# Optimization experiments

Measured on AMD Instinct MI355X. Metric: run time of the kernel, lower is better.

The kernel has to match this reference:

```python
import jax, jax.numpy as jnp
import numpy as np
import math

S = 72; IMG_W = 640; IMG_H = 360; STRIDE = 16
IN_CH = 256; AFC = 64
FMAP_H = IMG_H // STRIDE  # 22
FMAP_W = IMG_W // STRIDE  # 40
N_OFFSETS = S
LEFT_ANGLES = [72., 60., 49., 39., 30., 22.]
RIGHT_ANGLES = [108., 120., 131., 141., 150., 158.]
BOTTOM_ANGLES = [165., 150., 141., 131., 120., 108., 100., 90., 80., 72., 60., 49., 39., 30., 15.]
BATCH = 8


def _gen_anchor(start, angle, cut):
    n = FMAP_H if cut else N_OFFSETS
    ys = np.linspace(1., 0., n)
    a = np.zeros(5 + n)
    sx, sy = start
    a[2] = 1. - sy
    a[3] = sx
    a[5:] = (sx + (1. - ys - 1. + sy) / math.tan(angle * math.pi / 180.)) * IMG_W
    return a


def _gen_side(angles, nb, x=None, y=None):
    if x is None:
        starts = [(xx, y) for xx in np.linspace(1., 0., nb)]
    else:
        starts = [(x, yy) for yy in np.linspace(1., 0., nb)]
    anc = np.stack([_gen_anchor(s, a, False) for s in starts for a in angles])
    cut = np.stack([_gen_anchor(s, a, True) for s in starts for a in angles])
    return anc, cut


def build_anchor_tables():
    la, lc = _gen_side(LEFT_ANGLES, 72, x=0.)
    ra, rc = _gen_side(RIGHT_ANGLES, 72, x=1.)
    ba, bc = _gen_side(BOTTOM_ANGLES, 128, y=1.)
    anchors = np.concatenate([la, ba, ra]).astype(np.float32)  # [P, 5+S]
    cuts = np.concatenate([lc, bc, rc])                        # [P, 5+fmap_h]
    xs = np.flip(np.round(cuts[:, 5:] / STRIDE), axis=1).astype(np.int64)
    cut_xs = np.clip(xs, 0, FMAP_W - 1).astype(np.int32)       # [P, fmap_h]
    invalid = (xs < 0) | (xs > FMAP_W)                         # faithful to original (> not >=)
    return anchors, cut_xs, invalid


def setup_inputs():
    key = jax.random.key(0)
    ks = jax.random.split(key, 6)
    anchors, cut_xs, invalid = build_anchor_tables()
    P = anchors.shape[0]  # 2784
    D = AFC * FMAP_H      # 1408
    s = 0.02
    return {
        "x": jax.random.normal(ks[0], (BATCH, IN_CH, FMAP_H, FMAP_W), jnp.float32),
        "conv_w": jax.random.normal(ks[1], (AFC, IN_CH), jnp.float32) * s,
        "conv_b": jnp.zeros((AFC,), jnp.float32),
        "att_w": jax.random.normal(ks[2], (P - 1, D), jnp.float32) * s,
        "att_b": jnp.zeros((P - 1,), jnp.float32),
        "cls_w": jax.random.normal(ks[3], (2, 2 * D), jnp.float32) * s,
        "cls_b": jnp.zeros((2,), jnp.float32),
        "so_w": jax.random.normal(ks[4], (1, 2 * D), jnp.float32) * s,
        "so_b": jnp.zeros((1,), jnp.float32),
        "reg_w": jax.random.normal(ks[5], (N_OFFSETS + 1, 2 * D), jnp.float32) * s,
        "reg_b": jnp.zeros((N_OFFSETS + 1,), jnp.float32),
        "anchors": jnp.asarray(anchors),
        "cut_xs": jnp.asarray(cut_xs),
        "invalid_mask": jnp.asarray(invalid),
    }


def reference(x, conv_w, conv_b, att_w, att_b, cls_w, cls_b, so_w, so_b, reg_w, reg_b, anchors, cut_xs, invalid_mask):
    B = x.shape[0]
    P, H = cut_xs.shape
    # 1x1 conv
    feat = jnp.einsum('bchw,oc->bohw', x, conv_w) + conv_b[None, :, None, None]
    # fused anchor feature gather: rois[b,p,c,h] = feat[b,c,h,cut_xs[p,h]]
    rois = feat[:, :, jnp.arange(H)[None, :], cut_xs]           # [B,C,P,H]
    rois = jnp.transpose(rois, (0, 2, 1, 3))                    # [B,P,C,H]
    rois = jnp.where(invalid_mask[None, :, None, :], 0., rois)
    D = rois.shape[2] * H
    baf = rois.reshape(B, P, D)
    scores = baf.reshape(B * P, D) @ att_w.T + att_b
    attention = jax.nn.softmax(scores, axis=1).reshape(B, P, P - 1)
    # off-diagonal scatter (replaces torch eye/nonzero trick): M[b,i,j]=attention[b,i,j'] for j!=i, diag 0
    i_idx = jnp.arange(P)[:, None]
    j_off = jnp.arange(P - 1)[None, :]
    tgt_j = jnp.where(j_off < i_idx, j_off, j_off + 1)          # [P,P-1]
    M = jnp.zeros((B, P, P), x.dtype).at[:, jnp.broadcast_to(i_idx, (P, P - 1)), tgt_j].set(attention)
    # (baf^T @ M^T)^T == M @ baf
    att_feats = jnp.einsum('bpq,bqd->bpd', M, baf)
    feats = jnp.concatenate([att_feats, baf], axis=2).reshape(B * P, 2 * D)
    cls = (feats @ cls_w.T + cls_b).reshape(B, P, 2)
    so = jax.nn.sigmoid(feats @ so_w.T + so_b).reshape(B, P, 1)
    reg = (feats @ reg_w.T + reg_b).reshape(B, P, N_OFFSETS + 1)
    anc = jnp.broadcast_to(anchors[None], (B, P, anchors.shape[1]))
    reg_proposals = jnp.concatenate([cls, (anc[:, :, 2:3] + so) * 0.5, anc[:, :, 3:4], anc[:, :, 4:] + reg], axis=2)
    return reg_proposals, M, feat
```

## Files before the change

### kernel.cpp

```cpp
#include <hip/hip_runtime.h>
#include <stdint.h>

#define PTOT 2784
#define PM1  2783
#define DDIM 1408
#define NB   8
#define ROWS 22272
#define KHEAD 2816
#define MROW 2816
#define BTROWS 1536

typedef __attribute__((ext_vector_type(8))) short bf16x8;
typedef __attribute__((ext_vector_type(4))) float f32x4;
typedef long i64f8;
typedef __attribute__((ext_vector_type(2))) long i64x2;

__device__ __forceinline__ short f2bf_rne(float x) {
    uint32_t u = __float_as_uint(x);
    u += 0x7fffu + ((u >> 16) & 1u);
    return (short)(u >> 16);
}
__device__ __forceinline__ float bf2f(short s) {
    return __uint_as_float((uint32_t)(unsigned short)s << 16);
}

__device__ __forceinline__ unsigned char f2e4m3(float x) {
    uint32_t u = __float_as_uint(x);
    uint32_t sgn = (u >> 24) & 0x80u;
    uint32_t ax = u & 0x7fffffffu;
    ax += 0x7ffffu + ((ax >> 20) & 1u);
    if (ax >= 0x43E80000u) return (unsigned char)(sgn | 0x7Eu);
    if (ax < 0x3C800000u) return (unsigned char)sgn;
    uint32_t e = (ax >> 23) - 120u;
    uint32_t m = (ax >> 20) & 7u;
    return (unsigned char)(sgn | (e << 3) | m);
}

__device__ __forceinline__ uint32_t kperm(uint32_t c) {
    return (c & ~63u) + (((c >> 3) & 3) << 4) + (((c >> 5) & 1) << 3) + (c & 7);
}

__device__ __forceinline__ void gld16(const void* g, void* l) {
    __builtin_amdgcn_global_load_lds(
        (const __attribute__((address_space(1))) void*)(uintptr_t)g,
        (__attribute__((address_space(3))) void*)(uint32_t)(uintptr_t)l,
        16, 0, 0);
}

#define VMW(N) asm volatile("s_waitcnt vmcnt(" #N ")" ::: "memory")

__global__ __launch_bounds__(256) void k_conv(
    const float* __restrict__ x, const float* __restrict__ w,
    const float* __restrict__ cb, float* __restrict__ feat) {
  __shared__ float xs[256 * 32];
  int b = blockIdx.x / 28;
  int t0 = (blockIdx.x % 28) * 32;
  int t = threadIdx.x;
  for (int i = t; i < 256 * 32; i += 256) {
    int c = i >> 5, pos = i & 31;
    int hw = t0 + pos;
    xs[i] = (hw < 880) ? x[((size_t)b * 256 + c) * 880 + hw] : 0.f;
  }
  __syncthreads();
  int o = t & 63, g = t >> 6;
  float acc[8];
#pragma unroll
  for (int pp = 0; pp < 8; ++pp) acc[pp] = cb[o];
  const float* wr = w + o * 256;
  for (int c = 0; c < 256; ++c) {
    float wv = wr[c];
#pragma unroll
    for (int pp = 0; pp < 8; ++pp) acc[pp] += wv * xs[c * 32 + g + pp * 4];
  }
#pragma unroll
  for (int pp = 0; pp < 8; ++pp) {
    int hw = t0 + g + pp * 4;
    if (hw < 880) feat[((size_t)b * 64 + o) * 880 + hw] = acc[pp];
  }
}

__global__ __launch_bounds__(256) void k_prep(
    const float* __restrict__ att_w, const float* __restrict__ cls_w,
    const float* __restrict__ so_w, const float* __restrict__ reg_w,
    const float* __restrict__ cls_b, const float* __restrict__ so_b,
    const float* __restrict__ reg_b,
    short* __restrict__ attw, short* __restrict__ wbf,
    float* __restrict__ bias80, float* __restrict__ M,
    unsigned char* __restrict__ Mbf8, unsigned char* __restrict__ bafT8,
    short* __restrict__ Msc) {
  const uint32_t n_attw = 2816u * DDIM;
  const uint32_t n_w = 80u * KHEAD;
  const uint32_t n_pa = (uint32_t)NB * MROW * 32;
  const uint32_t n_pb = (uint32_t)NB * BTROWS * 32;
  const uint32_t total = n_attw + n_w + 80 + ROWS + n_pa + n_pb;
  for (uint32_t i = blockIdx.x * 256 + threadIdx.x; i < total;
       i += gridDim.x * 256) {
    if (i < n_attw) {
      uint32_t j = i / DDIM, k = i - j * DDIM;
      float v = (j < PM1) ? att_w[(size_t)j * DDIM + k] : 0.f;
      attw[i] = f2bf_rne(v);
    } else if (i < n_attw + n_w) {
      uint32_t ii = i - n_attw;
      uint32_t n = ii / KHEAD, k = ii - n * KHEAD;
      float v = 0.f;
      if (n < 2) v = cls_w[n * KHEAD + k];
      else if (n == 2) v = so_w[k];
      else if (n < 76) v = reg_w[(size_t)(n - 3) * KHEAD + k];
      wbf[ii] = f2bf_rne(v);
    } else if (i < n_attw + n_w + 80) {
      uint32_t n = i - n_attw - n_w;
      float v = 0.f;
      if (n < 2) v = cls_b[n];
      else if (n == 2) v = so_b[0];
      else if (n < 76) v = reg_b[n - 3];
      bias80[n] = v;
    } else if (i < n_attw + n_w + 80 + ROWS) {
      uint32_t r = i - n_attw - n_w - 80;
      uint32_t p = r % PTOT;
      M[(size_t)r * PTOT + p] = -1e30f;
      if (Msc) Msc[(size_t)r * PTOT + p] = f2bf_rne(-1e30f);
    } else if (i < n_attw + n_w + 80 + ROWS + n_pa) {
      uint32_t ii = i - n_attw - n_w - 80 - ROWS;
      uint32_t row = ii >> 5; uint32_t c = ii & 31;
      Mbf8[(size_t)row * 2816 + kperm(2784 + c)] = 0;
    } else {
      uint32_t ii = i - n_attw - n_w - 80 - ROWS - n_pa;
      uint32_t row = ii >> 5; uint32_t c = ii & 31;
      bafT8[(size_t)row * 2816 + kperm(2784 + c)] = 0;
    }
  }
}

__global__ __launch_bounds__(256) void k_gather(
    const float* __restrict__ feat, const int* __restrict__ cutx,
    const unsigned char* __restrict__ inval,
    short* __restrict__ baf, unsigned char* __restrict__ bafT8) {
  int p0 = blockIdx.x * 64, d0 = blockIdx.y * 64, b = blockIdx.z;
  __shared__ short tile[64][72];
  int t = threadIdx.x;
  for (int i = t; i < 64 * 64; i += 256) {
    int pl = i >> 6, dl = i & 63;
    int p = p0 + pl, d = d0 + dl;
    float v = 0.f;
    if (p < PTOT && d < DDIM) {
      int c = d / 22, h = d - c * 22;
      if (!inval[p * 22 + h]) {
        int xc = cutx[p * 22 + h];
        v = feat[(((size_t)b * 64 + c) * 22 + h) * 40 + xc];
      }
    }
    tile[pl][dl] = f2bf_rne(v);
  }
  __syncthreads();
  if (d0 < DDIM) {
    for (int u = t; u < 512; u += 256) {
      int pl = u >> 3, dg = u & 7;
      int p = p0 + pl;
      if (p < PTOT) {
        bf16x8 v;
#pragma unroll
        for (int e = 0; e < 8; ++e) v[e] = tile[pl][dg * 8 + e];
        *(bf16x8*)&baf[((size_t)b * PTOT + p) * DDIM + d0 + dg * 8] = v;
      }
    }
  }
  for (int u = t; u < 512; u += 256) {
    int dl = u >> 3, pg = u & 7;
    int pbase = p0 + pg * 8;
    if (pbase + 7 < PTOT) {
      unsigned long long pk = 0;
#pragma unroll
      for (int e = 0; e < 8; ++e) {
        float fv = bf2f(tile[pg * 8 + e][dl]);
        pk |= (unsigned long long)f2e4m3(fv) << (8 * e);
      }
      *(unsigned long long*)&bafT8[((size_t)b * BTROWS + d0 + dl) * 2816 +
                                   kperm(pbase)] = pk;
    }
  }
}

#define SC_TILE(OFF_, S_, SN_, STAGE_, VM_)                                    \
  {                                                                            \
    const char* cb_ = sm + (S_) * 24576;                                       \
    if (STAGE_) {                                                              \
      char* nb_ = sm + (SN_) * 24576;                                          \
      gld16(gA0 + (OFF_), nb_ + ddA);                                          \
      gld16(gB0 + (OFF_), nb_ + 8192 + ddA);                                   \
      gld16(gB1 + (OFF_), nb_ + 16384 + ddA);                                  \
    }                                                                          \
    if ((VM_) == 6) VMW(6); else if ((VM_) == 3) VMW(3); else VMW(0);          \
    __builtin_amdgcn_s_barrier();                                              \
    bf16x8 av[4], bv[4];                                                       \
    _Pragma("unroll") for (int i = 0; i < 4; ++i)                              \
      av[i] = *(const bf16x8*)(cb_ + offA[i]);                                 \
    _Pragma("unroll") for (int i = 0; i < 4; ++i)                              \
      bv[i] = *(const bf16x8*)(cb_ + 8192 + offB[i]);                          \
    __builtin_amdgcn_s_setprio(1);                                             \
    _Pragma("unroll") for (int mi = 0; mi < 4; ++mi)                           \
      _Pragma("unroll") for (int ni = 0; ni < 4; ++ni)                         \
        acc[mi][ni] = __builtin_amdgcn_mfma_f32_16x16x32_bf16(                 \
            av[mi], bv[ni], acc[mi][ni], 0, 0, 0);                             \
    __builtin_amdgcn_s_setprio(0);                                             \
    __builtin_amdgcn_s_barrier();                                              \
  }

template<int OUTMODE>
__global__ __launch_bounds__(512, 4) void k_scores(
    const short* __restrict__ baf, const short* __restrict__ attw,
    const float* __restrict__ att_b, float* __restrict__ Mout,
    short* __restrict__ Msc) {
  __shared__ char sm[73728];
  int wg = blockIdx.x;
  int xcd = wg & 7, lin = wg >> 3;
  int wgid = (xcd < 2) ? xcd * 240 + lin : 480 + (xcd - 2) * 239 + lin;
  int it = wgid / 11, nt = wgid - it * 11;
  int m0 = it * 128, n0 = nt * 256;

  int t = threadIdx.x, w = t >> 6, l = t & 63;
  int lr = l & 15, lg = l >> 4;
  int wr = w >> 2, wc = w & 3;

  const char* gA0; const char* gB0; const char* gB1;
  int ddA = t * 16;
  {
    int oA = t * 16;
    int rA = oA >> 6, cA = (oA & 63) ^ (((oA >> 7) & 3) << 4);
    gA0 = (const char*)(baf + (size_t)(m0 + rA) * DDIM) + cA;
    int oB0 = t * 16;
    int rB0 = oB0 >> 6, cB0 = (oB0 & 63) ^ (((oB0 >> 7) & 3) << 4);
    gB0 = (const char*)(attw + (size_t)(n0 + rB0) * DDIM) + cB0;
    int oB1 = 8192 + t * 16;
    int rB1 = oB1 >> 6, cB1 = (oB1 & 63) ^ (((oB1 >> 7) & 3) << 4);
    gB1 = (const char*)(attw + (size_t)(n0 + rB1) * DDIM) + cB1;
  }
  int offA[4], offB[4];
#pragma unroll
  for (int i = 0; i < 4; ++i) {
    int xa = (wr * 64 + i * 16 + lr) * 64 + lg * 16;
    offA[i] = xa ^ (((xa >> 7) & 3) << 4);
    int xb = (wc * 64 + i * 16 + lr) * 64 + lg * 16;
    offB[i] = xb ^ (((xb >> 7) & 3) << 4);
  }

  f32x4 acc[4][4];
  const f32x4 fz = {0.f, 0.f, 0.f, 0.f};
#pragma unroll
  for (int mi = 0; mi < 4; ++mi)
#pragma unroll
    for (int ni = 0; ni < 4; ++ni) acc[mi][ni] = fz;

  gld16(gA0, sm + ddA);
  gld16(gB0, sm + 8192 + ddA);
  gld16(gB1, sm + 16384 + ddA);
  gld16(gA0 + 64, sm + 24576 + ddA);
  gld16(gB0 + 64, sm + 24576 + 8192 + ddA);
  gld16(gB1 + 64, sm + 24576 + 16384 + ddA);

  for (int q = 0; q < 14; ++q) {
    SC_TILE(128, 0, 2, 1, 6);
    SC_TILE(192, 1, 0, 1, 6);
    SC_TILE(256, 2, 1, 1, 6);
    gA0 += 192; gB0 += 192; gB1 += 192;
  }
  SC_TILE(0, 0, 0, 0, 3);
  SC_TILE(0, 1, 0, 0, 0);

#pragma unroll
  for (int mi = 0; mi < 4; ++mi) {
#pragma unroll
    for (int rg = 0; rg < 4; ++rg) {
      int gmi = m0 + wr * 64 + mi * 16 + lg * 4 + rg;
      int i = gmi % PTOT;
#pragma unroll
      for (int ni = 0; ni < 4; ++ni) {
        int j = n0 + wc * 64 + ni * 16 + lr;
        if (j < PM1) {
          int q2 = j + (j >= i);
          float v = acc[mi][ni][rg] + att_b[j];
          if (OUTMODE == 0) Mout[(size_t)gmi * PTOT + q2] = v;
          else              Msc[(size_t)gmi * PTOT + q2] = f2bf_rne(v);
        }
      }
    }
  }
}

#define AF_TILE(OFF_, S_, SN_, STAGE_, VM_)                                    \
  {                                                                            \
    const char* cb_ = sm + (S_) * 24576;                                       \
    if (STAGE_) {                                                              \
      char* nb_ = sm + (SN_) * 24576;                                          \
      gld16(gA0 + (OFF_), nb_ + ddA);                                          \
      gld16(gB0 + (OFF_), nb_ + 8192 + ddA);                                   \
      gld16(gB1 + (OFF_), nb_ + 16384 + ddA);                                  \
    }                                                                          \
    if ((VM_) == 6) VMW(6); else if ((VM_) == 3) VMW(3); else VMW(0);          \
    __builtin_amdgcn_s_barrier();                                              \
    i64x2 aw[4], bw[4];                                                        \
    _Pragma("unroll") for (int i = 0; i < 4; ++i)                              \
      aw[i] = *(const i64x2*)(cb_ + offA[i]);                                  \
    _Pragma("unroll") for (int i = 0; i < 4; ++i)                              \
      bw[i] = *(const i64x2*)(cb_ + 8192 + offB[i]);                           \
    __builtin_amdgcn_s_setprio(1);                                             \
    _Pragma("unroll") for (int ks = 0; ks < 2; ++ks)                           \
      _Pragma("unroll") for (int mi = 0; mi < 4; ++mi)                         \
        _Pragma("unroll") for (int ni = 0; ni < 4; ++ni)                       \
          acc[mi][ni] = __builtin_amdgcn_mfma_f32_16x16x32_fp8_fp8(            \
              aw[mi][ks], bw[ni][ks], acc[mi][ni], 0, 0, 0);                   \
    __builtin_amdgcn_s_setprio(0);                                             \
    __builtin_amdgcn_s_barrier();                                              \
  }

__global__ __launch_bounds__(512, 4) void k_attfeat8(
    const unsigned char* __restrict__ Mbf8,
    const unsigned char* __restrict__ bafT8,
    short* __restrict__ attf) {
  __shared__ char sm[73728];
  int wg = blockIdx.x;
  int wgid = (wg & 7) * 132 + (wg >> 3);
  int bb = wgid / 132;
  int rem = wgid - bb * 132;
  int it = rem / 6, dt = rem - it * 6;
  int m0 = it * 128, n0 = dt * 256;
  const unsigned char* Ab = Mbf8 + ((size_t)bb * MROW + m0) * 2816;
  const unsigned char* Bb = bafT8 + ((size_t)bb * BTROWS + n0) * 2816;

  int t = threadIdx.x, w = t >> 6, l = t & 63;
  int lr = l & 15, lg = l >> 4;
  int wr = w >> 2, wc = w & 3;

  const char* gA0; const char* gB0; const char* gB1;
  int ddA = t * 16;
  {
    int oA = t * 16;
    int rA = oA >> 6, cA = (oA & 63) ^ (((oA >> 7) & 3) << 4);
    gA0 = (const char*)Ab + (size_t)rA * 2816 + cA;
    int oB0 = t * 16;
    int rB0 = oB0 >> 6, cB0 = (oB0 & 63) ^ (((oB0 >> 7) & 3) << 4);
    gB0 = (const char*)Bb + (size_t)rB0 * 2816 + cB0;
    int oB1 = 8192 + t * 16;
    int rB1 = oB1 >> 6, cB1 = (oB1 & 63) ^ (((oB1 >> 7) & 3) << 4);
    gB1 = (const char*)Bb + (size_t)rB1 * 2816 + cB1;
  }
  int offA[4], offB[4];
#pragma unroll
  for (int i = 0; i < 4; ++i) {
    int xa = (wr * 64 + i * 16 + lr) * 64 + lg * 16;
    offA[i] = xa ^ (((xa >> 7) & 3) << 4);
    int xb = (wc * 64 + i * 16 + lr) * 64 + lg * 16;
    offB[i] = xb ^ (((xb >> 7) & 3) << 4);
  }

  f32x4 acc[4][4];
  const f32x4 fz = {0.f, 0.f, 0.f, 0.f};
#pragma unroll
  for (int mi = 0; mi < 4; ++mi)
#pragma unroll
    for (int ni = 0; ni < 4; ++ni) acc[mi][ni] = fz;

  gld16(gA0, sm + ddA);
  gld16(gB0, sm + 8192 + ddA);
  gld16(gB1, sm + 16384 + ddA);
  gld16(gA0 + 64, sm + 24576 + ddA);
  gld16(gB0 + 64, sm + 24576 + 8192 + ddA);
  gld16(gB1 + 64, sm + 24576 + 16384 + ddA);

  for (int q = 0; q < 14; ++q) {
    AF_TILE(128, 0, 2, 1, 6);
    AF_TILE(192, 1, 0, 1, 6);
    AF_TILE(256, 2, 1, 1, 6);
    gA0 += 192; gB0 += 192; gB1 += 192;
  }
  AF_TILE(0, 0, 0, 0, 3);
  AF_TILE(0, 1, 0, 0, 0);

  const float US = 1.0f / 1024.0f;
#pragma unroll
  for (int mi = 0; mi < 4; ++mi) {
#pragma unroll
    for (int rg = 0; rg < 4; ++rg) {
      int i = m0 + wr * 64 + mi * 16 + lg * 4 + rg;
      if (i < PTOT) {
        short* arow = attf + ((size_t)(bb * PTOT + i)) * DDIM;
#pragma unroll
        for (int ni = 0; ni < 4; ++ni) {
          int d = n0 + wc * 64 + ni * 16 + lr;
          if (d < DDIM) arow[d] = f2bf_rne(acc[mi][ni][rg] * US);
        }
      }
    }
  }
}

template<int INMODE>
__global__ __launch_bounds__(256) void k_softmax(float* __restrict__ M,
                                                 unsigned char* __restrict__ Mbf8,
                                                 const short* __restrict__ Msc) {
  __shared__ float red[8];
  int r = blockIdx.x;
  int b = r / PTOT, p = r - b * PTOT;
  float* pr = M + (size_t)r * PTOT;
  const short* ms = INMODE ? (Msc + (size_t)r * PTOT) : (const short*)nullptr;
  unsigned char* mb = Mbf8 + ((size_t)b * MROW + p) * 2816;
  int t = threadIdx.x;
  bool has2 = (t < 348 - 256);
  float v0[8], v1[8];
  float mx = -3.0e38f;
  if (INMODE == 0) {
    f32x4 a0 = *(const f32x4*)(pr + t * 8);
    f32x4 a1 = *(const f32x4*)(pr + t * 8 + 4);
#pragma unroll
    for (int e = 0; e < 4; ++e) { v0[e] = a0[e]; v0[4 + e] = a1[e]; }
  } else {
    bf16x8 a = *(const bf16x8*)(ms + t * 8);
#pragma unroll
    for (int e = 0; e < 8; ++e) v0[e] = bf2f(a[e]);
  }
#pragma unroll
  for (int e = 0; e < 8; ++e) mx = fmaxf(mx, v0[e]);
  if (has2) {
    if (INMODE == 0) {
      f32x4 b0 = *(const f32x4*)(pr + (256 + t) * 8);
      f32x4 b1 = *(const f32x4*)(pr + (256 + t) * 8 + 4);
#pragma unroll
      for (int e = 0; e < 4; ++e) { v1[e] = b0[e]; v1[4 + e] = b1[e]; }
    } else {
      bf16x8 bb = *(const bf16x8*)(ms + (256 + t) * 8);
#pragma unroll
      for (int e = 0; e < 8; ++e) v1[e] = bf2f(bb[e]);
    }
#pragma unroll
    for (int e = 0; e < 8; ++e) mx = fmaxf(mx, v1[e]);
  }
#pragma unroll
  for (int off = 32; off; off >>= 1) mx = fmaxf(mx, __shfl_xor(mx, off));
  if ((t & 63) == 0) red[t >> 6] = mx;
  __syncthreads();
  mx = fmaxf(fmaxf(red[0], red[1]), fmaxf(red[2], red[3]));
  float s = 0.f;
#pragma unroll
  for (int e = 0; e < 8; ++e) { v0[e] = __expf(v0[e] - mx); s += v0[e]; }
  if (has2) {
#pragma unroll
    for (int e = 0; e < 8; ++e) { v1[e] = __expf(v1[e] - mx); s += v1[e]; }
  }
#pragma unroll
  for (int off = 32; off; off >>= 1) s += __shfl_xor(s, off);
  if ((t & 63) == 0) red[4 + (t >> 6)] = s;
  __syncthreads();
  s = (red[4] + red[5]) + (red[6] + red[7]);
  float inv = 1.f / s;
  float invs = inv * 1024.f;
  {
    f32x4 o0, o1; unsigned long long pk = 0;
#pragma unroll
    for (int e = 0; e < 8; ++e) {
      float wv = v0[e] * inv;
      if (e < 4) o0[e] = wv; else o1[e - 4] = wv;
      pk |= (unsigned long long)f2e4m3(v0[e] * invs) << (8 * e);
    }
    *(f32x4*)(pr + t * 8) = o0;
    *(f32x4*)(pr + t * 8 + 4) = o1;
    *(unsigned long long*)(mb + kperm((uint32_t)t * 8)) = pk;
  }
  if (has2) {
    f32x4 o0, o1; unsigned long long pk = 0;
#pragma unroll
    for (int e = 0; e < 8; ++e) {
      float wv = v1[e] * inv;
      if (e < 4) o0[e] = wv; else o1[e - 4] = wv;
      pk |= (unsigned long long)f2e4m3(v1[e] * invs) << (8 * e);
    }
    *(f32x4*)(pr + (256 + t) * 8) = o0;
    *(f32x4*)(pr + (256 + t) * 8 + 4) = o1;
    *(unsigned long long*)(mb + kperm((uint32_t)(256 + t) * 8)) = pk;
  }
}

__global__ __launch_bounds__(256) void k_head(
    const short* __restrict__ attf, const short* __restrict__ baf,
    const short* __restrict__ wbf, const float* __restrict__ bias80,
    const float* __restrict__ anch, float* __restrict__ out) {
  __shared__ char sm[27648];
  int r0 = blockIdx.x * 64;
  int t = threadIdx.x, w = t >> 6, lane = t & 63;
  int lr = lane & 15, lg = lane >> 4;
  int ddA = t * 16;
  const char* gA_att = (const char*)(attf + (size_t)(r0 + (t >> 2)) * DDIM) + (t & 3) * 16;
  const char* gA_baf = (const char*)(baf + (size_t)(r0 + (t >> 2)) * DDIM) + (t & 3) * 16;
  const char* gB1 = (const char*)(wbf + (size_t)(t >> 2) * KHEAD) + (t & 3) * 16;
  const char* gB2 = (const char*)(wbf + (size_t)(64 + (t >> 2)) * KHEAD) + (t & 3) * 16;
  int pAo = (w * 16 + lr) * 64 + lg * 16;
  int pBo = 4096 + lr * 64 + lg * 16;
  f32x4 acc[5];
  const f32x4 fz = {0.f, 0.f, 0.f, 0.f};
#pragma unroll
  for (int i2 = 0; i2 < 5; ++i2) acc[i2] = fz;

#pragma unroll
  for (int s = 0; s < 2; ++s) {
    char* nb = sm + s * 9216;
    gld16(gA_att + s * 64, nb + ddA);
    gld16(gB1 + s * 64, nb + 4096 + ddA);
    if (t < 64) gld16(gB2 + s * 64, nb + 8192 + ddA);
  }

#pragma unroll
  for (int kt = 0; kt < 88; ++kt) {
    const char* cb_ = sm + (kt % 3) * 9216;
    int s = kt + 2;
    if (s < 88) {
      char* nb_ = sm + (s % 3) * 9216;
      const char* asrc = (s < 44) ? (gA_att + s * 64) : (gA_baf + (s - 44) * 64);
      gld16(asrc, nb_ + ddA);
      gld16(gB1 + s * 64, nb_ + 4096 + ddA);
      if (t < 64) gld16(gB2 + s * 64, nb_ + 8192 + ddA);
    }
    if (w == 0) { if (kt < 86) VMW(6); else if (kt == 86) VMW(3); else VMW(0); }
    else        { if (kt < 86) VMW(4); else if (kt == 86) VMW(2); else VMW(0); }
    __builtin_amdgcn_s_barrier();
    bf16x8 a = *(const bf16x8*)(cb_ + pAo);
    __builtin_amdgcn_s_setprio(1);
#pragma unroll
    for (int ni = 0; ni < 5; ++ni) {
      bf16x8 bvv = *(const bf16x8*)(cb_ + pBo + ni * 1024);
      acc[ni] = __builtin_amdgcn_mfma_f32_16x16x32_bf16(a, bvv, acc[ni], 0, 0, 0);
    }
    __builtin_amdgcn_s_setprio(0);
    __builtin_amdgcn_s_barrier();
  }

#pragma unroll
  for (int ni = 0; ni < 5; ++ni) {
#pragma unroll
    for (int rg = 0; rg < 4; ++rg) {
      int n = ni * 16 + lr;
      int i = w * 16 + lg * 4 + rg;
      int rgl = r0 + i;
      int p = rgl % PTOT;
      float v = acc[ni][rg] + bias80[n];
      if (n < 2) {
        out[(size_t)rgl * 77 + n] = v;
      } else if (n == 2) {
        out[(size_t)rgl * 77 + 2] =
            (anch[(size_t)p * 77 + 2] + 1.f / (1.f + __expf(-v))) * 0.5f;
        out[(size_t)rgl * 77 + 3] = anch[(size_t)p * 77 + 3];
      } else if (n < 76) {
        out[(size_t)rgl * 77 + n + 1] = v + anch[(size_t)p * 77 + n + 1];
      }
    }
  }
}

extern "C" void kernel_launch(void* const* d_in, const int* in_sizes, int n_in,
                              void* d_out, int out_size, void* d_ws, size_t ws_size,
                              hipStream_t stream) {
  const float* x      = (const float*)d_in[0];
  const float* conv_w = (const float*)d_in[1];
  const float* conv_b = (const float*)d_in[2];
  const float* att_w  = (const float*)d_in[3];
  const float* att_b  = (const float*)d_in[4];
  const float* cls_w  = (const float*)d_in[5];
  const float* cls_b  = (const float*)d_in[6];
  const float* so_w   = (const float*)d_in[7];
  const float* so_b   = (const float*)d_in[8];
  const float* reg_w  = (const float*)d_in[9];
  const float* reg_b  = (const float*)d_in[10];
  const float* anchors= (const float*)d_in[11];
  const int*   cut_xs = (const int*)d_in[12];
  const unsigned char* invalid = (const unsigned char*)d_in[13];

  float* out_rp = (float*)d_out;
  float* Mmat = out_rp + (size_t)ROWS * 77;
  float* feat = Mmat + (size_t)ROWS * PTOT;

  char* wsp = (char*)d_ws;
  short* baf            = (short*)wsp;
  unsigned char* bafT8  = (unsigned char*)(wsp + 62717952ULL);
  unsigned char* Mbf8   = (unsigned char*)(wsp + 97320960ULL);
  short* attw           = (short*)(wsp + 160759808ULL);
  short* wbf            = (short*)(wsp + 168689664ULL);
  float* bias80         = (float*)(wsp + 169140224ULL);
  short* attf           = (short*)(wsp + 169140736ULL);
  short* Msc            = (short*)(wsp + 231858688ULL);
  const size_t WS_FAST  = 231858688ULL + 124010496ULL;

  bool fast = (ws_size >= WS_FAST);

  k_conv<<<224, 256, 0, stream>>>(x, conv_w, conv_b, feat);
  k_prep<<<2048, 256, 0, stream>>>(att_w, cls_w, so_w, reg_w, cls_b, so_b, reg_b,
                                   attw, wbf, bias80, Mmat, Mbf8, bafT8,
                                   fast ? Msc : (short*)nullptr);
  k_gather<<<dim3(44, 24, 8), 256, 0, stream>>>(feat, cut_xs, invalid, baf, bafT8);
  if (fast) {
    k_scores<1><<<1914, 512, 0, stream>>>(baf, attw, att_b, (float*)nullptr, Msc);
    k_softmax<1><<<ROWS, 256, 0, stream>>>(Mmat, Mbf8, Msc);
  } else {
    k_scores<0><<<1914, 512, 0, stream>>>(baf, attw, att_b, Mmat, (short*)nullptr);
    k_softmax<0><<<ROWS, 256, 0, stream>>>(Mmat, Mbf8, (const short*)nullptr);
  }
  k_attfeat8<<<1056, 512, 0, stream>>>(Mbf8, bafT8, attf);
  k_head<<<348, 256, 0, stream>>>(attf, baf, wbf, bias80, anchors, out_rp);
}
```

Before: 608.1 us.

## Load A operand directly from global into registers in scores GEMM

The baf (A) tile in the attention-scores GEMM is now read straight from global memory into registers, one K-step ahead, instead of being staged through shared memory. Only the attw (B) tile still goes through LDS, which shrinks the shared buffer from 72KB to 48KB and drops the A-side LDS reads. The aim is to cut LDS traffic and footprint. In exchange each wave now issues uncoalesced per-row 16-byte global loads, which A-rows are not shared across the four column waves that reuse them, and the vmcnt wait counts now have to cover both load types.

Result: slower. 1.275 ms (+109.7%).

```diff
diff --git a/kernel.cpp b/kernel.cpp
--- a/kernel.cpp
+++ b/kernel.cpp
@@ -180,29 +180,34 @@
   }
 }
 
-#define SC_TILE(OFF_, S_, SN_, STAGE_, VM_)                                    \
+#define SC_TILE(BOFF_, AOFF_, S_, SN_, STAGE_, LOADA_, VM_)                    \
   {                                                                            \
-    const char* cb_ = sm + (S_) * 24576;                                       \
+    const char* cb_ = sm + (S_) * 16384;                                       \
+    bf16x8 awn[4];                                                             \
+    if (LOADA_) {                                                              \
+      _Pragma("unroll") for (int i = 0; i < 4; ++i)                            \
+        awn[i] = *(const bf16x8*)(gAr[i] + (AOFF_));                           \
+    }                                                                          \
     if (STAGE_) {                                                              \
-      char* nb_ = sm + (SN_) * 24576;                                          \
-      gld16(gA0 + (OFF_), nb_ + ddA);                                          \
-      gld16(gB0 + (OFF_), nb_ + 8192 + ddA);                                   \
-      gld16(gB1 + (OFF_), nb_ + 16384 + ddA);                                  \
+      char* nb_ = sm + (SN_) * 16384;                                          \
+      gld16(gB0 + (BOFF_), nb_ + ddA);                                         \
+      gld16(gB1 + (BOFF_), nb_ + 8192 + ddA);                                  \
     }                                                                          \
-    if ((VM_) == 6) VMW(6); else if ((VM_) == 3) VMW(3); else VMW(0);          \
+    if ((VM_) == 8) VMW(8); else if ((VM_) == 6) VMW(6); else VMW(0);          \
     __builtin_amdgcn_s_barrier();                                              \
-    bf16x8 av[4], bv[4];                                                       \
+    bf16x8 bv[4];                                                              \
     _Pragma("unroll") for (int i = 0; i < 4; ++i)                              \
-      av[i] = *(const bf16x8*)(cb_ + offA[i]);                                 \
-    _Pragma("unroll") for (int i = 0; i < 4; ++i)                              \
-      bv[i] = *(const bf16x8*)(cb_ + 8192 + offB[i]);                          \
+      bv[i] = *(const bf16x8*)(cb_ + offB[i]);                                 \
     __builtin_amdgcn_s_setprio(1);                                             \
     _Pragma("unroll") for (int mi = 0; mi < 4; ++mi)                           \
       _Pragma("unroll") for (int ni = 0; ni < 4; ++ni)                         \
         acc[mi][ni] = __builtin_amdgcn_mfma_f32_16x16x32_bf16(                 \
-            av[mi], bv[ni], acc[mi][ni], 0, 0, 0);                             \
+            aw[mi], bv[ni], acc[mi][ni], 0, 0, 0);                             \
     __builtin_amdgcn_s_setprio(0);                                             \
     __builtin_amdgcn_s_barrier();                                              \
+    if (LOADA_) {                                                              \
+      _Pragma("unroll") for (int i = 0; i < 4; ++i) aw[i] = awn[i];            \
+    }                                                                          \
   }
 
 template<int OUTMODE>
@@ -210,7 +215,7 @@
     const short* __restrict__ baf, const short* __restrict__ attw,
     const float* __restrict__ att_b, float* __restrict__ Mout,
     short* __restrict__ Msc) {
-  __shared__ char sm[73728];
+  __shared__ char sm[49152];
   int wg = blockIdx.x;
   int xcd = wg & 7, lin = wg >> 3;
   int wgid = (xcd < 2) ? xcd * 240 + lin : 480 + (xcd - 2) * 239 + lin;
@@ -221,12 +226,9 @@
   int lr = l & 15, lg = l >> 4;
   int wr = w >> 2, wc = w & 3;
 
-  const char* gA0; const char* gB0; const char* gB1;
+  const char* gB0; const char* gB1;
   int ddA = t * 16;
   {
-    int oA = t * 16;
-    int rA = oA >> 6, cA = (oA & 63) ^ (((oA >> 7) & 3) << 4);
-    gA0 = (const char*)(baf + (size_t)(m0 + rA) * DDIM) + cA;
     int oB0 = t * 16;
     int rB0 = oB0 >> 6, cB0 = (oB0 & 63) ^ (((oB0 >> 7) & 3) << 4);
     gB0 = (const char*)(attw + (size_t)(n0 + rB0) * DDIM) + cB0;
@@ -234,14 +236,17 @@
     int rB1 = oB1 >> 6, cB1 = (oB1 & 63) ^ (((oB1 >> 7) & 3) << 4);
     gB1 = (const char*)(attw + (size_t)(n0 + rB1) * DDIM) + cB1;
   }
-  int offA[4], offB[4];
+  int offB[4];
 #pragma unroll
   for (int i = 0; i < 4; ++i) {
-    int xa = (wr * 64 + i * 16 + lr) * 64 + lg * 16;
-    offA[i] = xa ^ (((xa >> 7) & 3) << 4);
     int xb = (wc * 64 + i * 16 + lr) * 64 + lg * 16;
     offB[i] = xb ^ (((xb >> 7) & 3) << 4);
   }
+  const char* gAr[4];
+#pragma unroll
+  for (int i = 0; i < 4; ++i)
+    gAr[i] = (const char*)(baf + (size_t)(m0 + wr * 64 + i * 16 + lr) * DDIM)
+             + lg * 16;
 
   f32x4 acc[4][4];
   const f32x4 fz = {0.f, 0.f, 0.f, 0.f};
@@ -250,21 +255,26 @@
 #pragma unroll
     for (int ni = 0; ni < 4; ++ni) acc[mi][ni] = fz;
 
-  gld16(gA0, sm + ddA);
-  gld16(gB0, sm + 8192 + ddA);
-  gld16(gB1, sm + 16384 + ddA);
-  gld16(gA0 + 64, sm + 24576 + ddA);
-  gld16(gB0 + 64, sm + 24576 + 8192 + ddA);
-  gld16(gB1 + 64, sm + 24576 + 16384 + ddA);
+  bf16x8 aw[4];
+#pragma unroll
+  for (int i = 0; i < 4; ++i) aw[i] = *(const bf16x8*)(gAr[i]);
+  gld16(gB0, sm + ddA);
+  gld16(gB1, sm + 8192 + ddA);
+  gld16(gB0 + 64, sm + 16384 + ddA);
+  gld16(gB1 + 64, sm + 16384 + 8192 + ddA);
+  VMW(2);
+  __builtin_amdgcn_s_barrier();
 
   for (int q = 0; q < 14; ++q) {
-    SC_TILE(128, 0, 2, 1, 6);
-    SC_TILE(192, 1, 0, 1, 6);
-    SC_TILE(256, 2, 1, 1, 6);
-    gA0 += 192; gB0 += 192; gB1 += 192;
-  }
-  SC_TILE(0, 0, 0, 0, 3);
-  SC_TILE(0, 1, 0, 0, 0);
+    SC_TILE(128, 64, 0, 2, 1, 1, 8);
+    SC_TILE(192, 128, 1, 0, 1, 1, 8);
+    SC_TILE(256, 192, 2, 1, 1, 1, 8);
+    gB0 += 192; gB1 += 192;
+#pragma unroll
+    for (int i = 0; i < 4; ++i) gAr[i] += 192;
+  }
+  SC_TILE(0, 64, 0, 0, 0, 1, 6);
+  SC_TILE(0, 0, 1, 0, 0, 0, 0);
 
 #pragma unroll
   for (int mi = 0; mi < 4; ++mi) {
```
